# Optimization experiments

Measured on AMD Instinct MI355X. Metric: run time of the kernel, lower is better.

Reference implementation:

```python
import jax, jax.numpy as jnp
import numpy as np

# Minifloat meta: fp8 e4m3-style (4 exponent bits, 3 mantissa bits, bias = 2^(E-1)-1)
EXP_BITS = 4
MAN_BITS = 3


def quantize_minifloat(t, exp_bits=EXP_BITS, man_bits=MAN_BITS):
    """Fake-quantize a float tensor to a minifloat grid (round-to-nearest, saturate).

    Simulates extract_minifloat_component + dequantize: snap each value to the
    nearest representable minifloat with `exp_bits` exponent bits and
    `man_bits` mantissa bits (IEEE-style bias, subnormals supported via the
    clamped minimum exponent, saturating clamp at max normal value).
    """
    bias = 2 ** (exp_bits - 1) - 1
    emin = 1 - bias                      # min normal exponent
    emax = bias                          # max exponent (no inf/nan specials)
    max_val = (2.0 - 2.0 ** (-man_bits)) * (2.0 ** emax)
    ax = jnp.abs(t)
    # exponent of each value; zeros are safe because 0/scale == 0
    e = jnp.floor(jnp.log2(jnp.where(ax > 0, ax, 1.0)))
    e = jnp.maximum(e, float(emin))      # flush into subnormal grid
    scale = jnp.exp2(e - man_bits)       # quantization step at this exponent
    q = jnp.round(t / scale) * scale
    return jnp.clip(q, -max_val, max_val)


def setup_inputs() -> dict:
    key = jax.random.key(0)
    k1, k2, k3 = jax.random.split(key, 3)
    tokens, d_in, d_out = 32768, 1024, 1024
    x = jax.random.normal(k1, (tokens, d_in), dtype=jnp.float32)
    w = jax.random.normal(k2, (d_out, d_in), dtype=jnp.float32) * 0.02
    b = jax.random.normal(k3, (d_out,), dtype=jnp.float32) * 0.02
    return {"x": x, "w": w, "b": b}


def reference(x, w, b):
    # layer_type 'XqWqBq': minifloat-quantize activations, weight and bias,
    # then fused linear: y = xq @ wq.T + bq   (nn.Linear convention, w: [out, in])
    xq = quantize_minifloat(x)
    wq = quantize_minifloat(w)
    bq = quantize_minifloat(b)
    return jnp.einsum("ti,oi->to", xq, wq) + bq
```

## Files before the change

kernel.cpp:

```cpp
#include <hip/hip_runtime.h>

typedef __bf16 bf16x8 __attribute__((ext_vector_type(8)));
typedef float f32x4 __attribute__((ext_vector_type(4)));

__device__ __forceinline__ float quant1(float t) {
    unsigned bits = __float_as_uint(t);
    int eb = (int)((bits & 0x7fffffffu) >> 23);
    eb = eb < 121 ? 121 : eb;
    float m = __uint_as_float((unsigned)(257 - eb) << 23);
    float s = __uint_as_float((unsigned)(eb - 3) << 23);
    float q = rintf(t * m) * s;
    q = fminf(q, 240.0f);
    q = fmaxf(q, -240.0f);
    return q;
}

__device__ __forceinline__ unsigned short bf16bits(float f) {
    return (unsigned short)(__float_as_uint(f) >> 16);
}

__global__ void quant8_bf16_kernel(const float* __restrict__ in,
                                   unsigned short* __restrict__ out, long long n8) {
    long long i = (long long)blockIdx.x * blockDim.x + threadIdx.x;
    if (i >= n8) return;
    const float4* p = (const float4*)in;
    float4 a = p[2 * i], b = p[2 * i + 1];
    union { unsigned short u[8]; uint4 v; } o;
    o.u[0] = bf16bits(quant1(a.x));
    o.u[1] = bf16bits(quant1(a.y));
    o.u[2] = bf16bits(quant1(a.z));
    o.u[3] = bf16bits(quant1(a.w));
    o.u[4] = bf16bits(quant1(b.x));
    o.u[5] = bf16bits(quant1(b.y));
    o.u[6] = bf16bits(quant1(b.z));
    o.u[7] = bf16bits(quant1(b.w));
    ((uint4*)out)[i] = o.v;
}

__global__ void quant_f32_kernel(const float* __restrict__ in,
                                 float* __restrict__ out, int n) {
    int i = blockIdx.x * blockDim.x + threadIdx.x;
    if (i < n) out[i] = quant1(in[i]);
}

#define BM 128
#define BN 128
#define BK 32

__device__ __forceinline__ void gload_lds16(const void* g, void* l) {
    __builtin_amdgcn_global_load_lds(
        (const __attribute__((address_space(1))) void*)g,
        (__attribute__((address_space(3))) void*)l, 16, 0, 0);
}

__global__ __launch_bounds__(256, 2) void gemm_bf16q_kernel(
    const unsigned short* __restrict__ A,
    const unsigned short* __restrict__ B,
    const float* __restrict__ bias,
    float* __restrict__ C, int M, int N, int K)
{
    __shared__ __align__(16) unsigned short As[BM * BK];
    __shared__ __align__(16) unsigned short Bs[BN * BK];

    const int t    = threadIdx.x;
    const int lane = t & 63;
    const int wid  = t >> 6;
    const int wm   = (wid >> 1) * 64;
    const int wn   = (wid & 1) * 64;
    const int fr   = lane & 15;
    const int kg   = lane >> 4;

    const int rowA0 = blockIdx.x * BM;
    const int colB0 = blockIdx.y * BN;

    f32x4 acc[4][4] = {};

    const int c0 = t;
    const int c1 = t + 256;

    for (int kt = 0; kt < K; kt += BK) {
        {
            const unsigned short* ga0 = A + (size_t)(rowA0 + (c0 >> 2)) * K + kt + (c0 & 3) * 8;
            gload_lds16(ga0, &As[c0 * 8]);
            const unsigned short* ga1 = A + (size_t)(rowA0 + (c1 >> 2)) * K + kt + (c1 & 3) * 8;
            gload_lds16(ga1, &As[c1 * 8]);
            const unsigned short* gb0 = B + (size_t)(colB0 + (c0 >> 2)) * K + kt + (c0 & 3) * 8;
            gload_lds16(gb0, &Bs[c0 * 8]);
            const unsigned short* gb1 = B + (size_t)(colB0 + (c1 >> 2)) * K + kt + (c1 & 3) * 8;
            gload_lds16(gb1, &Bs[c1 * 8]);
        }
        __syncthreads();

        bf16x8 af[4], bfm[4];
        #pragma unroll
        for (int m = 0; m < 4; ++m)
            af[m] = *(const bf16x8*)&As[(wm + m * 16 + fr) * BK + kg * 8];
        #pragma unroll
        for (int n = 0; n < 4; ++n)
            bfm[n] = *(const bf16x8*)&Bs[(wn + n * 16 + fr) * BK + kg * 8];

        #pragma unroll
        for (int m = 0; m < 4; ++m)
            #pragma unroll
            for (int n = 0; n < 4; ++n)
                acc[m][n] = __builtin_amdgcn_mfma_f32_16x16x32_bf16(
                    af[m], bfm[n], acc[m][n], 0, 0, 0);

        __syncthreads();
    }

    #pragma unroll
    for (int m = 0; m < 4; ++m) {
        int row = rowA0 + wm + m * 16 + kg * 4;
        #pragma unroll
        for (int n = 0; n < 4; ++n) {
            int col = colB0 + wn + n * 16 + fr;
            float bb = bias[col];
            #pragma unroll
            for (int r = 0; r < 4; ++r)
                C[(size_t)(row + r) * N + col] = acc[m][n][r] + bb;
        }
    }
}

__global__ void naive_gemm_kernel(const float* __restrict__ x, const float* __restrict__ w,
                                  const float* __restrict__ b, float* __restrict__ out,
                                  int M, int N, int K) {
    int col = blockIdx.x * blockDim.x + threadIdx.x;
    int row = blockIdx.y;
    if (col >= N || row >= M) return;
    const float* xr = x + (size_t)row * K;
    const float* wr = w + (size_t)col * K;
    float acc = 0.f;
    for (int k = 0; k < K; ++k) acc += quant1(xr[k]) * quant1(wr[k]);
    out[(size_t)row * N + col] = acc + quant1(b[col]);
}

extern "C" void kernel_launch(void* const* d_in, const int* in_sizes, int n_in,
                              void* d_out, int out_size, void* d_ws, size_t ws_size,
                              hipStream_t stream) {
    const float* x = (const float*)d_in[0];
    const float* w = (const float*)d_in[1];
    const float* b = (const float*)d_in[2];
    float* out = (float*)d_out;

    const int xsz = in_sizes[0];
    const int wsz = in_sizes[1];
    const int N   = in_sizes[2];
    const int K   = wsz / N;
    const int M   = xsz / K;

    const size_t xq_bytes = (size_t)xsz * 2;
    const size_t wq_bytes = (size_t)wsz * 2;
    const size_t need = xq_bytes + wq_bytes + (size_t)N * 4;

    const bool fast_ok = (ws_size >= need) &&
                         (M % BM == 0) && (N % BN == 0) && (K % BK == 0) &&
                         (xsz % 8 == 0) && (wsz % 8 == 0);

    if (fast_ok) {
        unsigned short* xq = (unsigned short*)d_ws;
        unsigned short* wq = (unsigned short*)((char*)d_ws + xq_bytes);
        float*          bq = (float*)((char*)d_ws + xq_bytes + wq_bytes);

        long long n8x = xsz / 8;
        quant8_bf16_kernel<<<(int)((n8x + 255) / 256), 256, 0, stream>>>(x, xq, n8x);
        long long n8w = wsz / 8;
        quant8_bf16_kernel<<<(int)((n8w + 255) / 256), 256, 0, stream>>>(w, wq, n8w);
        quant_f32_kernel<<<(N + 255) / 256, 256, 0, stream>>>(b, bq, N);

        dim3 grid(M / BM, N / BN);
        gemm_bf16q_kernel<<<grid, 256, 0, stream>>>(xq, wq, bq, out, M, N, K);
    } else {
        dim3 grid((N + 255) / 256, M);
        naive_gemm_kernel<<<grid, 256, 0, stream>>>(x, w, b, out, M, N, K);
    }
}
```

Baseline: 316.5 us.

## Quantize operands to fp8 e4m3 bytes and use fp8 MFMA GEMM

```diff
diff --git a/kernel.cpp b/kernel.cpp
--- a/kernel.cpp
+++ b/kernel.cpp
@@ -1,6 +1,5 @@
 #include <hip/hip_runtime.h>
 
-typedef __bf16 bf16x8 __attribute__((ext_vector_type(8)));
 typedef float f32x4 __attribute__((ext_vector_type(4)));
 
 __device__ __forceinline__ float quant1(float t) {
@@ -15,37 +14,40 @@
     return q;
 }
 
-__device__ __forceinline__ unsigned short bf16bits(float f) {
-    return (unsigned short)(__float_as_uint(f) >> 16);
+__device__ __forceinline__ unsigned fp8q1(float t) {
+    float q = quant1(t);
+    unsigned qb = __float_as_uint(q);
+    unsigned sg = (qb >> 24) & 0x80u;
+    unsigned aq = qb & 0x7fffffffu;
+    unsigned e2 = aq >> 23;
+    unsigned sub = (unsigned)(int)(__uint_as_float(aq) * 512.0f);
+    unsigned nrm = ((e2 - 120u) << 3) | ((qb >> 20) & 7u);
+    unsigned mag = (aq == 0u) ? 0u : (e2 >= 121u ? nrm : sub);
+    return sg | mag;
 }
 
-__global__ void quant8_bf16_kernel(const float* __restrict__ in,
-                                   unsigned short* __restrict__ out, long long n8) {
-    long long i = (long long)blockIdx.x * blockDim.x + threadIdx.x;
-    if (i >= n8) return;
-    const float4* p = (const float4*)in;
-    float4 a = p[2 * i], b = p[2 * i + 1];
-    union { unsigned short u[8]; uint4 v; } o;
-    o.u[0] = bf16bits(quant1(a.x));
-    o.u[1] = bf16bits(quant1(a.y));
-    o.u[2] = bf16bits(quant1(a.z));
-    o.u[3] = bf16bits(quant1(a.w));
-    o.u[4] = bf16bits(quant1(b.x));
-    o.u[5] = bf16bits(quant1(b.y));
-    o.u[6] = bf16bits(quant1(b.z));
-    o.u[7] = bf16bits(quant1(b.w));
-    ((uint4*)out)[i] = o.v;
-}
-
-__global__ void quant_f32_kernel(const float* __restrict__ in,
-                                 float* __restrict__ out, int n) {
-    int i = blockIdx.x * blockDim.x + threadIdx.x;
-    if (i < n) out[i] = quant1(in[i]);
+__global__ void quant8_fp8_kernel(const float* __restrict__ x, const float* __restrict__ w,
+                                  unsigned char* __restrict__ xq, unsigned char* __restrict__ wq,
+                                  long long n8x, long long n8tot) {
+    long long stride = (long long)gridDim.x * blockDim.x;
+    for (long long c = (long long)blockIdx.x * blockDim.x + threadIdx.x;
+         c < n8tot; c += stride) {
+        const float4* src;
+        unsigned char* dst;
+        long long i;
+        if (c < n8x) { src = (const float4*)x; dst = xq; i = c; }
+        else         { src = (const float4*)w; dst = wq; i = c - n8x; }
+        float4 a = src[2 * i], b = src[2 * i + 1];
+        unsigned lo = fp8q1(a.x) | (fp8q1(a.y) << 8) | (fp8q1(a.z) << 16) | (fp8q1(a.w) << 24);
+        unsigned hi = fp8q1(b.x) | (fp8q1(b.y) << 8) | (fp8q1(b.z) << 16) | (fp8q1(b.w) << 24);
+        uint2 o; o.x = lo; o.y = hi;
+        ((uint2*)dst)[i] = o;
+    }
 }
 
 #define BM 128
 #define BN 128
-#define BK 32
+#define BKF 64
 
 __device__ __forceinline__ void gload_lds16(const void* g, void* l) {
     __builtin_amdgcn_global_load_lds(
@@ -53,14 +55,14 @@
         (__attribute__((address_space(3))) void*)l, 16, 0, 0);
 }
 
-__global__ __launch_bounds__(256, 2) void gemm_bf16q_kernel(
-    const unsigned short* __restrict__ A,
-    const unsigned short* __restrict__ B,
+__global__ __launch_bounds__(256, 2) void gemm_fp8q_kernel(
+    const unsigned char* __restrict__ A,
+    const unsigned char* __restrict__ B,
     const float* __restrict__ bias,
     float* __restrict__ C, int M, int N, int K)
 {
-    __shared__ __align__(16) unsigned short As[BM * BK];
-    __shared__ __align__(16) unsigned short Bs[BN * BK];
+    __shared__ __align__(16) unsigned char As[BM * BKF];
+    __shared__ __align__(16) unsigned char Bs[BN * BKF];
 
     const int t    = threadIdx.x;
     const int lane = t & 63;
@@ -77,34 +79,36 @@
 
     const int c0 = t;
     const int c1 = t + 256;
+    const int r0 = c0 >> 2, j0 = (c0 & 3) * 16;
+    const int r1 = c1 >> 2, j1 = (c1 & 3) * 16;
 
-    for (int kt = 0; kt < K; kt += BK) {
-        {
-            const unsigned short* ga0 = A + (size_t)(rowA0 + (c0 >> 2)) * K + kt + (c0 & 3) * 8;
-            gload_lds16(ga0, &As[c0 * 8]);
-            const unsigned short* ga1 = A + (size_t)(rowA0 + (c1 >> 2)) * K + kt + (c1 & 3) * 8;
-            gload_lds16(ga1, &As[c1 * 8]);
-            const unsigned short* gb0 = B + (size_t)(colB0 + (c0 >> 2)) * K + kt + (c0 & 3) * 8;
-            gload_lds16(gb0, &Bs[c0 * 8]);
-            const unsigned short* gb1 = B + (size_t)(colB0 + (c1 >> 2)) * K + kt + (c1 & 3) * 8;
-            gload_lds16(gb1, &Bs[c1 * 8]);
-        }
+    for (int kt = 0; kt < K; kt += BKF) {
+        gload_lds16(A + (size_t)(rowA0 + r0) * K + kt + j0, &As[c0 * 16]);
+        gload_lds16(A + (size_t)(rowA0 + r1) * K + kt + j1, &As[c1 * 16]);
+        gload_lds16(B + (size_t)(colB0 + r0) * K + kt + j0, &Bs[c0 * 16]);
+        gload_lds16(B + (size_t)(colB0 + r1) * K + kt + j1, &Bs[c1 * 16]);
         __syncthreads();
 
-        bf16x8 af[4], bfm[4];
+        long af[4][2], bf[4][2];
         #pragma unroll
         for (int m = 0; m < 4; ++m)
-            af[m] = *(const bf16x8*)&As[(wm + m * 16 + fr) * BK + kg * 8];
+            #pragma unroll
+            for (int s = 0; s < 2; ++s)
+                af[m][s] = *(const long*)&As[(wm + m * 16 + fr) * BKF + s * 32 + kg * 8];
         #pragma unroll
         for (int n = 0; n < 4; ++n)
-            bfm[n] = *(const bf16x8*)&Bs[(wn + n * 16 + fr) * BK + kg * 8];
+            #pragma unroll
+            for (int s = 0; s < 2; ++s)
+                bf[n][s] = *(const long*)&Bs[(wn + n * 16 + fr) * BKF + s * 32 + kg * 8];
 
         #pragma unroll
         for (int m = 0; m < 4; ++m)
             #pragma unroll
             for (int n = 0; n < 4; ++n)
-                acc[m][n] = __builtin_amdgcn_mfma_f32_16x16x32_bf16(
-                    af[m], bfm[n], acc[m][n], 0, 0, 0);
+                #pragma unroll
+                for (int s = 0; s < 2; ++s)
+                    acc[m][n] = __builtin_amdgcn_mfma_f32_16x16x32_fp8_fp8(
+                        af[m][s], bf[n][s], acc[m][n], 0, 0, 0);
 
         __syncthreads();
     }
@@ -115,7 +119,7 @@
         #pragma unroll
         for (int n = 0; n < 4; ++n) {
             int col = colB0 + wn + n * 16 + fr;
-            float bb = bias[col];
+            float bb = quant1(bias[col]);
             #pragma unroll
             for (int r = 0; r < 4; ++r)
                 C[(size_t)(row + r) * N + col] = acc[m][n][r] + bb;
@@ -150,27 +154,23 @@
     const int K   = wsz / N;
     const int M   = xsz / K;
 
-    const size_t xq_bytes = (size_t)xsz * 2;
-    const size_t wq_bytes = (size_t)wsz * 2;
-    const size_t need = xq_bytes + wq_bytes + (size_t)N * 4;
+    const size_t xq_bytes = (size_t)xsz;
+    const size_t need = xq_bytes + (size_t)wsz;
 
     const bool fast_ok = (ws_size >= need) &&
-                         (M % BM == 0) && (N % BN == 0) && (K % BK == 0) &&
+                         (M % BM == 0) && (N % BN == 0) && (K % BKF == 0) &&
                          (xsz % 8 == 0) && (wsz % 8 == 0);
 
     if (fast_ok) {
-        unsigned short* xq = (unsigned short*)d_ws;
-        unsigned short* wq = (unsigned short*)((char*)d_ws + xq_bytes);
-        float*          bq = (float*)((char*)d_ws + xq_bytes + wq_bytes);
+        unsigned char* xq = (unsigned char*)d_ws;
+        unsigned char* wq = (unsigned char*)d_ws + xq_bytes;
 
         long long n8x = xsz / 8;
-        quant8_bf16_kernel<<<(int)((n8x + 255) / 256), 256, 0, stream>>>(x, xq, n8x);
-        long long n8w = wsz / 8;
-        quant8_bf16_kernel<<<(int)((n8w + 255) / 256), 256, 0, stream>>>(w, wq, n8w);
-        quant_f32_kernel<<<(N + 255) / 256, 256, 0, stream>>>(b, bq, N);
+        long long n8tot = n8x + wsz / 8;
+        quant8_fp8_kernel<<<2048, 256, 0, stream>>>(x, w, xq, wq, n8x, n8tot);
 
         dim3 grid(M / BM, N / BN);
-        gemm_bf16q_kernel<<<grid, 256, 0, stream>>>(xq, wq, bq, out, M, N, K);
+        gemm_fp8q_kernel<<<grid, 256, 0, stream>>>(xq, wq, b, out, M, N, K);
     } else {
         dim3 grid((N + 255) / 256, M);
         naive_gemm_kernel<<<grid, 256, 0, stream>>>(x, w, b, out, M, N, K);
```

Result: slower. 354.0 us (+11.9%).
